# Kernel optimization log

Measured on AMD Instinct MI355X. Metric: run time of the kernel, lower is better.

The kernel has to match this reference:

```python
import jax, jax.numpy as jnp
import numpy as np

B, S, D = 4, 2048, 1024
H, HD = 16, 64
DFF = 4096
EPS = 1e-6


def setup_inputs() -> dict:
    key = jax.random.key(0)
    ks = jax.random.split(key, 16)
    sc = 0.02
    def w(k, shape):
        return jax.random.normal(k, shape, dtype=jnp.float32) * sc
    return {
        'x': jax.random.normal(ks[0], (B, S, D), dtype=jnp.float32),
        'wq': w(ks[1], (D, D)), 'bq': jnp.zeros((D,), jnp.float32),
        'wk': w(ks[2], (D, D)), 'bk': jnp.zeros((D,), jnp.float32),
        'wv': w(ks[3], (D, D)), 'bv': jnp.zeros((D,), jnp.float32),
        'wo': w(ks[4], (D, D)), 'bo': jnp.zeros((D,), jnp.float32),
        'w1': w(ks[5], (D, DFF)), 'b1': jnp.zeros((DFF,), jnp.float32),
        'w2': w(ks[6], (DFF, D)), 'b2': jnp.zeros((D,), jnp.float32),
        'ln1_a': jnp.ones((D,), jnp.float32), 'ln1_b': jnp.zeros((D,), jnp.float32),
        'ln2_a': jnp.ones((D,), jnp.float32), 'ln2_b': jnp.zeros((D,), jnp.float32),
    }


def layernorm(x, alpha, bias):
    # Matches torch module: std is unbiased (ddof=1), divide by (std + eps)
    mean = jnp.mean(x, axis=-1, keepdims=True)
    var = jnp.sum((x - mean) ** 2, axis=-1, keepdims=True) / (x.shape[-1] - 1)
    std = jnp.sqrt(var)
    return alpha * ((x - mean) / (std + EPS)) + bias


def mha(x, wq, bq, wk, bk, wv, bv, wo, bo):
    q = (x @ wq + bq).reshape(B, S, H, HD)
    k = (x @ wk + bk).reshape(B, S, H, HD)
    v = (x @ wv + bv).reshape(B, S, H, HD)
    scores = jnp.einsum('bqhd,bkhd->bhqk', q, k) / jnp.sqrt(jnp.float32(HD))
    attn = jax.nn.softmax(scores, axis=-1)
    out = jnp.einsum('bhqk,bkhd->bqhd', attn, v).reshape(B, S, D)
    return out @ wo + bo


def reference(x, wq, bq, wk, bk, wv, bv, wo, bo, w1, b1, w2, b2,
              ln1_a, ln1_b, ln2_a, ln2_b):
    # Residual 1: x + MHA(LN(x))   (dropout = identity, eval mode)
    x = x + mha(layernorm(x, ln1_a, ln1_b), wq, bq, wk, bk, wv, bv, wo, bo)
    # Residual 2: x + FFN(LN(x))
    h = layernorm(x, ln2_a, ln2_b)
    ffn = jax.nn.relu(h @ w1 + b1) @ w2 + b2
    return x + ffn
```

## Files before the change

kernel.cpp:

```cpp
#include <hip/hip_runtime.h>

#define S_ 2048
#define D_ 1024

typedef unsigned short u16;
typedef unsigned int u32;
typedef __bf16 bf16x8 __attribute__((ext_vector_type(8)));
typedef unsigned short us8 __attribute__((ext_vector_type(8)));
typedef unsigned short us4 __attribute__((ext_vector_type(4)));
typedef unsigned int u32x4 __attribute__((ext_vector_type(4)));
typedef float f32x4 __attribute__((ext_vector_type(4)));

#if __has_builtin(__builtin_amdgcn_exp2f)
#define EXP2(x) __builtin_amdgcn_exp2f(x)
#else
#define EXP2(x) exp2f(x)
#endif

static __device__ __forceinline__ u16 f2bf(float f) {
  unsigned u = __builtin_bit_cast(unsigned, f);
  u += 0x7fffu + ((u >> 16) & 1u);
  return (u16)(u >> 16);
}

static __device__ __forceinline__ unsigned cvtpk_bf16(float lo, float hi) {
  unsigned r;
  asm("v_cvt_pk_bf16_f32 %0, %1, %2" : "=v"(r) : "v"(lo), "v"(hi));
  return r;
}

static __device__ __forceinline__ f32x4 mfma16(bf16x8 a, bf16x8 b, f32x4 c) {
  return __builtin_amdgcn_mfma_f32_16x16x32_bf16(a, b, c, 0, 0, 0);
}

static __device__ __forceinline__ void gload16(const void* g, void* lds) {
  __builtin_amdgcn_global_load_lds((const __attribute__((address_space(1))) void*)g,
                                   (__attribute__((address_space(3))) void*)lds, 16, 0, 0);
}

__global__ __launch_bounds__(256) void wtrans_kernel(const float* __restrict__ in,
                                                     u16* __restrict__ out, int K, int N,
                                                     float scale) {
  __shared__ float t[32][33];
  const int n0 = blockIdx.x * 32, k0 = blockIdx.y * 32;
  const int tx = threadIdx.x, ty = threadIdx.y;
#pragma unroll
  for (int i = 0; i < 4; i++)
    t[ty + 8 * i][tx] = in[(size_t)(k0 + ty + 8 * i) * N + n0 + tx];
  __syncthreads();
#pragma unroll
  for (int i = 0; i < 4; i++)
    out[(size_t)(n0 + ty + 8 * i) * K + k0 + tx] = f2bf(t[tx][ty + 8 * i] * scale);
}

__global__ __launch_bounds__(256) void bcat_kernel(const float* __restrict__ bq,
                                                   const float* __restrict__ bk,
                                                   const float* __restrict__ bv,
                                                   float* __restrict__ out, float qs) {
  const int i = blockIdx.x * 256 + threadIdx.x;
  out[i] = (i < 1024) ? bq[i] * qs : ((i < 2048) ? bk[i - 1024] : bv[i - 2048]);
}

__global__ __launch_bounds__(256) void ln_kernel(const float* __restrict__ in,
                                                 u16* __restrict__ out,
                                                 const float* __restrict__ alpha,
                                                 const float* __restrict__ beta) {
  const int row = blockIdx.x;
  const int tid = threadIdx.x;
  const float4 v = *(const float4*)(in + (size_t)row * D_ + tid * 4);
  float s = v.x + v.y + v.z + v.w;
  float ss = v.x * v.x + v.y * v.y + v.z * v.z + v.w * v.w;
#pragma unroll
  for (int off = 32; off >= 1; off >>= 1) {
    s += __shfl_xor(s, off);
    ss += __shfl_xor(ss, off);
  }
  __shared__ float red[8];
  const int w = tid >> 6, lane = tid & 63;
  if (lane == 0) { red[w] = s; red[4 + w] = ss; }
  __syncthreads();
  s = red[0] + red[1] + red[2] + red[3];
  ss = red[4] + red[5] + red[6] + red[7];
  const float mean = s * (1.0f / D_);
  const float var = (ss - s * mean) * (1.0f / (D_ - 1));
  const float inv = 1.0f / (sqrtf(var) + 1e-6f);
  const int j = tid * 4;
  const float4 av = *(const float4*)(alpha + j);
  const float4 bv = *(const float4*)(beta + j);
  us4 o;
  o[0] = f2bf((v.x - mean) * inv * av.x + bv.x);
  o[1] = f2bf((v.y - mean) * inv * av.y + bv.y);
  o[2] = f2bf((v.z - mean) * inv * av.z + bv.z);
  o[3] = f2bf((v.w - mean) * inv * av.w + bv.w);
  *(us4*)(out + (size_t)row * D_ + j) = o;
}

template <int OM, bool RELU, bool RESID>
__global__ __launch_bounds__(512, 2) void gemm_bt(const u16* __restrict__ A,
                                                  const u16* __restrict__ Bt,
                                                  const float* __restrict__ bias,
                                                  const float* __restrict__ resid,
                                                  void* __restrict__ outp,
                                                  void* __restrict__ out1,
                                                  void* __restrict__ out2, int N, int K) {
  __shared__ u16 lds[3 * 24576];
  const int tid = threadIdx.x;
  const int lane = tid & 63, w = tid >> 6;
  const int g = lane >> 4, r = lane & 15;
  const int wr = w >> 1, wc = w & 1;
  const size_t row0 = (size_t)blockIdx.y * 256;
  const int col0 = blockIdx.x * 128;

  float bias4[4];
#pragma unroll
  for (int n = 0; n < 4; n++) bias4[n] = bias[col0 + wc * 64 + n * 16 + r];

  f32x4 acc[4][4];
#pragma unroll
  for (int m = 0; m < 4; m++)
#pragma unroll
    for (int n = 0; n < 4; n++) {
      f32x4 z = {bias4[n], bias4[n], bias4[n], bias4[n]};
      acc[m][n] = z;
    }

  const int lrow = w * 8 + (lane >> 3);
  const int scol = 8 * ((lane & 7) ^ (lane >> 3));
  const u16* gA = A + (row0 + lrow) * (size_t)K + scol;
  const u16* gB = Bt + ((size_t)col0 + lrow) * (size_t)K + scol;
  const int nt = K >> 6;
  const int sw = (r & 7) << 3;

  int bufi = 0;
#pragma unroll
  for (int t0 = 0; t0 < 2; t0++) {
    u16* dA = lds + t0 * 24576 + w * 512;
#pragma unroll
    for (int j = 0; j < 4; j++) gload16(gA + (size_t)(j * 64) * K + t0 * 64, dA + j * 4096);
#pragma unroll
    for (int j = 0; j < 2; j++)
      gload16(gB + (size_t)(j * 64) * K + t0 * 64, dA + 16384 + j * 4096);
  }

  for (int t = 0; t < nt; ++t) {
    if (t + 1 < nt)
      asm volatile("s_waitcnt vmcnt(6)" ::: "memory");
    else
      asm volatile("s_waitcnt vmcnt(0)" ::: "memory");
    __builtin_amdgcn_s_barrier();
    asm volatile("" ::: "memory");
    if (t + 2 < nt) {
      const int tn = t + 2;
      const int bn = (bufi + 2 >= 3) ? bufi - 1 : bufi + 2;
      u16* dA = lds + bn * 24576 + w * 512;
      const size_t ko = (size_t)tn * 64;
#pragma unroll
      for (int j = 0; j < 4; j++) gload16(gA + (size_t)(j * 64) * K + ko, dA + j * 4096);
#pragma unroll
      for (int j = 0; j < 2; j++) gload16(gB + (size_t)(j * 64) * K + ko, dA + 16384 + j * 4096);
    }
    const u16* As_ = lds + bufi * 24576;
    const u16* Bs_ = As_ + 16384;
    bf16x8 af[2][4], bfr[2][4];
#pragma unroll
    for (int kk = 0; kk < 2; kk++) {
#pragma unroll
      for (int m = 0; m < 4; m++)
        af[kk][m] = __builtin_bit_cast(
            bf16x8, *(const us8*)(As_ + (wr * 64 + m * 16 + r) * 64 + ((kk * 32 + g * 8) ^ sw)));
#pragma unroll
      for (int n = 0; n < 4; n++)
        bfr[kk][n] = __builtin_bit_cast(
            bf16x8, *(const us8*)(Bs_ + (wc * 64 + n * 16 + r) * 64 + ((kk * 32 + g * 8) ^ sw)));
    }
    __builtin_amdgcn_s_setprio(1);
#pragma unroll
    for (int m = 0; m < 4; m++)
#pragma unroll
      for (int n = 0; n < 4; n++) {
        acc[m][n] = mfma16(af[0][m], bfr[0][n], acc[m][n]);
        acc[m][n] = mfma16(af[1][m], bfr[1][n], acc[m][n]);
      }
    __builtin_amdgcn_s_setprio(0);
    bufi = (bufi == 2) ? 0 : bufi + 1;
  }

#pragma unroll
  for (int m = 0; m < 4; m++)
#pragma unroll
    for (int n = 0; n < 4; n++) {
      if (OM == 2) {
        const int seg = col0 >> 10;
        const int cl = (col0 & 1023) + wc * 64 + n * 16 + r;
        if (seg == 2) {
          const int head = cl >> 6, hd = cl & 63;
          const size_t rg0 = row0 + wr * 64 + m * 16 + 4 * g;
          const int b = (int)(rg0 >> 11), s0 = (int)(rg0 & 2047);
          us4 o;
#pragma unroll
          for (int i = 0; i < 4; i++) o[i] = f2bf(acc[m][n][i]);
          *(us4*)((u16*)out2 + (((size_t)(b * 16 + head) * 64 + hd) * S_ + s0)) = o;
        } else {
          u16* dst = (u16*)(seg == 0 ? outp : out1);
#pragma unroll
          for (int i = 0; i < 4; i++) {
            const size_t rg = row0 + wr * 64 + m * 16 + 4 * g + i;
            dst[rg * D_ + cl] = f2bf(acc[m][n][i]);
          }
        }
      } else {
#pragma unroll
        for (int i = 0; i < 4; i++) {
          const size_t rg = row0 + wr * 64 + m * 16 + 4 * g + i;
          const int cg = col0 + wc * 64 + n * 16 + r;
          float v = acc[m][n][i];
          if (RESID) v += resid[rg * N + cg];
          if (RELU) v = fmaxf(v, 0.0f);
          if (OM == 1)
            ((float*)outp)[rg * N + cg] = v;
          else
            ((u16*)outp)[rg * N + cg] = f2bf(v);
        }
      }
    }
}

__global__ __launch_bounds__(256) void attn_kernel(const u16* __restrict__ Q,
                                                   const u16* __restrict__ Km,
                                                   const u16* __restrict__ Vt_g,
                                                   u16* __restrict__ O) {
  __shared__ u16 Klds[64 * 64];
  __shared__ u16 Vlds[64 * 68];
  const int tid = threadIdx.x;
  const int lane = tid & 63, w = tid >> 6;
  const int g = lane >> 4, r = lane & 15;
  const int bh = blockIdx.y;
  const int b = bh >> 4, head = bh & 15;
  const size_t rowbase = (size_t)b * S_;
  const int colbase = head * 64;
  const int q0 = blockIdx.x * 64 + w * 16;

  const u16* qrow = Q + (rowbase + q0 + r) * D_ + colbase;
  const bf16x8 qf0 = __builtin_bit_cast(bf16x8, *(const us8*)(qrow + g * 8));
  const bf16x8 qf1 = __builtin_bit_cast(bf16x8, *(const us8*)(qrow + 32 + g * 8));

  const int srow = tid >> 3;
  const int sslot = (tid & 7) ^ (srow & 7);
  const u16* Kg = Km + (rowbase + srow) * D_ + colbase + sslot * 8;
  const u16* Vg = Vt_g + ((size_t)bh * 64 + srow) * S_ + (tid & 7) * 8;
  char* lK = (char*)Klds + w * 1024;

  float l_run = 0.0f;
  f32x4 oacc[4];
#pragma unroll
  for (int n = 0; n < 4; n++) {
    f32x4 z = {0.0f, 0.0f, 0.0f, 0.0f};
    oacc[n] = z;
  }

  for (int kt = 0; kt < S_ / 64; kt++) {
    const us8 v0 = *(const us8*)(Vg + (size_t)kt * 64);
    const us8 v1 = *(const us8*)(Vg + 32 * S_ + (size_t)kt * 64);
    __syncthreads();
    gload16(Kg + (size_t)kt * 64 * D_, lK);
    gload16(Kg + (size_t)(kt * 64 + 32) * D_, lK + 4096);
    *(us8*)(Vlds + srow * 68 + (tid & 7) * 8) = v0;
    *(us8*)(Vlds + (srow + 32) * 68 + (tid & 7) * 8) = v1;
    __syncthreads();

    f32x4 st[4];
    __builtin_amdgcn_s_setprio(1);
#pragma unroll
    for (int f = 0; f < 4; f++) {
      const int row = f * 16 + r;
      const int sw = row & 7;
      const bf16x8 k0 = __builtin_bit_cast(bf16x8, *(const us8*)(Klds + row * 64 + (g ^ sw) * 8));
      const bf16x8 k1 =
          __builtin_bit_cast(bf16x8, *(const us8*)(Klds + row * 64 + ((g + 4) ^ sw) * 8));
      f32x4 z = {0.0f, 0.0f, 0.0f, 0.0f};
      st[f] = mfma16(k0, qf0, z);
      st[f] = mfma16(k1, qf1, st[f]);
    }
    __builtin_amdgcn_s_setprio(0);
    u32 pw[8];
#pragma unroll
    for (int f = 0; f < 4; f++) {
      const float e0 = EXP2(st[f][0]);
      const float e1 = EXP2(st[f][1]);
      const float e2 = EXP2(st[f][2]);
      const float e3 = EXP2(st[f][3]);
      l_run += (e0 + e1) + (e2 + e3);
      pw[f * 2] = cvtpk_bf16(e0, e1);
      pw[f * 2 + 1] = cvtpk_bf16(e2, e3);
    }

    const u32x4 a0w = {pw[0], pw[1], pw[2], pw[3]};
    const u32x4 a1w = {pw[4], pw[5], pw[6], pw[7]};
    const bf16x8 a0 = __builtin_bit_cast(bf16x8, a0w);
    const bf16x8 a1 = __builtin_bit_cast(bf16x8, a1w);
    __builtin_amdgcn_s_setprio(1);
#pragma unroll
    for (int n = 0; n < 4; n++) {
      const u16* vr = Vlds + (n * 16 + r) * 68;
      const us4 v00 = *(const us4*)(vr + g * 4);
      const us4 v01 = *(const us4*)(vr + 16 + g * 4);
      const us4 v10 = *(const us4*)(vr + 32 + g * 4);
      const us4 v11 = *(const us4*)(vr + 48 + g * 4);
      const bf16x8 vb0 =
          __builtin_bit_cast(bf16x8, __builtin_shufflevector(v00, v01, 0, 1, 2, 3, 4, 5, 6, 7));
      const bf16x8 vb1 =
          __builtin_bit_cast(bf16x8, __builtin_shufflevector(v10, v11, 0, 1, 2, 3, 4, 5, 6, 7));
      oacc[n] = mfma16(a0, vb0, oacc[n]);
      oacc[n] = mfma16(a1, vb1, oacc[n]);
    }
    __builtin_amdgcn_s_setprio(0);
  }

  l_run += __shfl_xor(l_run, 16);
  l_run += __shfl_xor(l_run, 32);
  float ld[4];
#pragma unroll
  for (int i = 0; i < 4; i++) ld[i] = 1.0f / __shfl(l_run, 4 * g + i);
#pragma unroll
  for (int n = 0; n < 4; n++)
#pragma unroll
    for (int i = 0; i < 4; i++)
      O[(rowbase + q0 + 4 * g + i) * D_ + colbase + n * 16 + r] = f2bf(oacc[n][i] * ld[i]);
}

extern "C" void kernel_launch(void* const* d_in, const int* in_sizes, int n_in, void* d_out,
                              int out_size, void* d_ws, size_t ws_size, hipStream_t stream) {
  (void)in_sizes; (void)n_in; (void)out_size; (void)ws_size;
  const float* x = (const float*)d_in[0];
  const float* wq = (const float*)d_in[1];
  const float* bq = (const float*)d_in[2];
  const float* wk = (const float*)d_in[3];
  const float* bk = (const float*)d_in[4];
  const float* wv = (const float*)d_in[5];
  const float* bv = (const float*)d_in[6];
  const float* wo = (const float*)d_in[7];
  const float* bo = (const float*)d_in[8];
  const float* w1 = (const float*)d_in[9];
  const float* b1 = (const float*)d_in[10];
  const float* w2 = (const float*)d_in[11];
  const float* b2 = (const float*)d_in[12];
  const float* ln1a = (const float*)d_in[13];
  const float* ln1b = (const float*)d_in[14];
  const float* ln2a = (const float*)d_in[15];
  const float* ln2b = (const float*)d_in[16];

  char* ws = (char*)d_ws;
  const size_t MB = 1ull << 20;
  u16* wqkv = (u16*)(ws + 0 * MB);
  u16* wqt = wqkv;
  u16* wkt = (u16*)(ws + 2 * MB);
  u16* wvt = (u16*)(ws + 4 * MB);
  u16* wot = (u16*)(ws + 6 * MB);
  u16* w1t = (u16*)(ws + 8 * MB);
  u16* w2t = (u16*)(ws + 16 * MB);
  u16* xA = (u16*)(ws + 24 * MB);
  u16* qb = (u16*)(ws + 40 * MB);
  u16* kb = (u16*)(ws + 56 * MB);
  u16* vt = (u16*)(ws + 72 * MB);
  float* bcat = (float*)(ws + 88 * MB);
  u16* ff1 = (u16*)(ws + 40 * MB);
  float* x1 = (float*)(ws + 104 * MB);

  const float QSCALE = 0.125f * 1.4426950408889634f;

  const dim3 tb(32, 8);
  wtrans_kernel<<<dim3(32, 32), tb, 0, stream>>>(wq, wqt, 1024, 1024, QSCALE);
  wtrans_kernel<<<dim3(32, 32), tb, 0, stream>>>(wk, wkt, 1024, 1024, 1.0f);
  wtrans_kernel<<<dim3(32, 32), tb, 0, stream>>>(wv, wvt, 1024, 1024, 1.0f);
  wtrans_kernel<<<dim3(32, 32), tb, 0, stream>>>(wo, wot, 1024, 1024, 1.0f);
  wtrans_kernel<<<dim3(128, 32), tb, 0, stream>>>(w1, w1t, 1024, 4096, 1.0f);
  wtrans_kernel<<<dim3(32, 128), tb, 0, stream>>>(w2, w2t, 4096, 1024, 1.0f);
  bcat_kernel<<<12, 256, 0, stream>>>(bq, bk, bv, bcat, QSCALE);

  ln_kernel<<<8192, 256, 0, stream>>>(x, xA, ln1a, ln1b);
  gemm_bt<2, false, false><<<dim3(24, 32), 512, 0, stream>>>(xA, wqkv, bcat, nullptr, qb, kb, vt,
                                                             3072, 1024);
  attn_kernel<<<dim3(32, 64), 256, 0, stream>>>(qb, kb, vt, xA);
  gemm_bt<1, false, true><<<dim3(8, 32), 512, 0, stream>>>(xA, wot, bo, x, x1, nullptr, nullptr,
                                                           1024, 1024);
  ln_kernel<<<8192, 256, 0, stream>>>(x1, xA, ln2a, ln2b);
  gemm_bt<0, true, false><<<dim3(32, 32), 512, 0, stream>>>(xA, w1t, b1, nullptr, ff1, nullptr,
                                                            nullptr, 4096, 1024);
  gemm_bt<1, false, true><<<dim3(8, 32), 512, 0, stream>>>(ff1, w2t, b2, x1, (float*)d_out,
                                                           nullptr, nullptr, 1024, 4096);
}
```

Baseline: 394.9 us.

## Interleave global prefetch with MFMA phases and remap workgroups for cache locality

Splits each K-tile's compute into four row phases. Each phase loads only its A fragments from LDS, and the global-to-LDS prefetch loads for the tile two steps ahead are spread across the phases so memory issue overlaps MFMA work. It also remaps the workgroup index with a stride-8 permutation so that neighbouring tiles share cache, likely aimed at the chiplet/XCD layout. In exchange it adds three intra-loop barriers and explicit lgkmcnt waits per tile, which could cause stalls.

```diff
diff --git a/kernel.cpp b/kernel.cpp
--- a/kernel.cpp
+++ b/kernel.cpp
@@ -108,8 +108,14 @@
   const int lane = tid & 63, w = tid >> 6;
   const int g = lane >> 4, r = lane & 15;
   const int wr = w >> 1, wc = w & 1;
-  const size_t row0 = (size_t)blockIdx.y * 256;
-  const int col0 = blockIdx.x * 128;
+
+  const int gx = gridDim.x;
+  const int nwg = gx * gridDim.y;
+  const int orig = blockIdx.y * gx + blockIdx.x;
+  const int nid = (orig & 7) * (nwg >> 3) + (orig >> 3);
+  const int bx = nid % gx, by = nid / gx;
+  const size_t row0 = (size_t)by * 256;
+  const int col0 = bx * 128;
 
   float bias4[4];
 #pragma unroll
@@ -149,39 +155,52 @@
       asm volatile("s_waitcnt vmcnt(0)" ::: "memory");
     __builtin_amdgcn_s_barrier();
     asm volatile("" ::: "memory");
-    if (t + 2 < nt) {
-      const int tn = t + 2;
-      const int bn = (bufi + 2 >= 3) ? bufi - 1 : bufi + 2;
-      u16* dA = lds + bn * 24576 + w * 512;
-      const size_t ko = (size_t)tn * 64;
-#pragma unroll
-      for (int j = 0; j < 4; j++) gload16(gA + (size_t)(j * 64) * K + ko, dA + j * 4096);
-#pragma unroll
-      for (int j = 0; j < 2; j++) gload16(gB + (size_t)(j * 64) * K + ko, dA + 16384 + j * 4096);
-    }
+    const bool st = (t + 2 < nt);
+    const int bn = (bufi + 2 >= 3) ? bufi - 1 : bufi + 2;
+    u16* dS = lds + bn * 24576 + w * 512;
+    const size_t ko = (size_t)(t + 2) * 64;
     const u16* As_ = lds + bufi * 24576;
     const u16* Bs_ = As_ + 16384;
-    bf16x8 af[2][4], bfr[2][4];
-#pragma unroll
-    for (int kk = 0; kk < 2; kk++) {
-#pragma unroll
-      for (int m = 0; m < 4; m++)
-        af[kk][m] = __builtin_bit_cast(
-            bf16x8, *(const us8*)(As_ + (wr * 64 + m * 16 + r) * 64 + ((kk * 32 + g * 8) ^ sw)));
-#pragma unroll
-      for (int n = 0; n < 4; n++)
-        bfr[kk][n] = __builtin_bit_cast(
-            bf16x8, *(const us8*)(Bs_ + (wc * 64 + n * 16 + r) * 64 + ((kk * 32 + g * 8) ^ sw)));
-    }
-    __builtin_amdgcn_s_setprio(1);
-#pragma unroll
-    for (int m = 0; m < 4; m++)
+    bf16x8 bfr[2][4];
+
+#pragma unroll
+    for (int p = 0; p < 4; ++p) {
+      bf16x8 a0 = __builtin_bit_cast(
+          bf16x8, *(const us8*)(As_ + (wr * 64 + p * 16 + r) * 64 + ((g * 8) ^ sw)));
+      bf16x8 a1 = __builtin_bit_cast(
+          bf16x8, *(const us8*)(As_ + (wr * 64 + p * 16 + r) * 64 + ((32 + g * 8) ^ sw)));
+      if (p == 0) {
+#pragma unroll
+        for (int kk = 0; kk < 2; kk++)
+#pragma unroll
+          for (int n = 0; n < 4; n++)
+            bfr[kk][n] = __builtin_bit_cast(
+                bf16x8,
+                *(const us8*)(Bs_ + (wc * 64 + n * 16 + r) * 64 + ((kk * 32 + g * 8) ^ sw)));
+      }
+      if (st) {
+        if (p == 0) {
+          gload16(gA + ko, dS);
+          gload16(gA + (size_t)64 * K + ko, dS + 4096);
+        } else if (p == 1) {
+          gload16(gA + (size_t)128 * K + ko, dS + 8192);
+          gload16(gA + (size_t)192 * K + ko, dS + 12288);
+        } else if (p == 2) {
+          gload16(gB + ko, dS + 16384);
+          gload16(gB + (size_t)64 * K + ko, dS + 20480);
+        }
+      }
+      asm volatile("s_waitcnt lgkmcnt(0)" ::: "memory");
+      __builtin_amdgcn_sched_barrier(0);
+      __builtin_amdgcn_s_setprio(1);
 #pragma unroll
       for (int n = 0; n < 4; n++) {
-        acc[m][n] = mfma16(af[0][m], bfr[0][n], acc[m][n]);
-        acc[m][n] = mfma16(af[1][m], bfr[1][n], acc[m][n]);
+        acc[p][n] = mfma16(a0, bfr[0][n], acc[p][n]);
+        acc[p][n] = mfma16(a1, bfr[1][n], acc[p][n]);
       }
-    __builtin_amdgcn_s_setprio(0);
+      __builtin_amdgcn_s_setprio(0);
+      if (p < 3) __builtin_amdgcn_s_barrier();
+    }
     bufi = (bufi == 2) ? 0 : bufi + 1;
   }
 
```

Measured after the change: 395.4 us. Within noise of the previous version (+0.1%).
